# Optimization experiments

Hardware: AMD Instinct MI355X
Metric: run time of the kernel (lower is better)

Reference implementation:

```python
import jax, jax.numpy as jnp
import numpy as np

N = 50000
E = 800000
IN_C, HID_C, OUT_C = 128, 256, 2


def sage_conv(x, src, dst, W_l, b_l, W_r, num_nodes):
    # PyG SAGEConv with mean aggregation:
    #   out = lin_l(mean_{j in N(i)} x_j) + lin_r(x_i)
    msg = x[src]                                            # [E, d] gather
    agg = jax.ops.segment_sum(msg, dst, num_segments=num_nodes)   # [N, d]
    cnt = jax.ops.segment_sum(jnp.ones((msg.shape[0],), x.dtype), dst,
                              num_segments=num_nodes)        # [N]
    agg = agg / jnp.maximum(cnt, 1.0)[:, None]               # mean (deg>=1)
    return agg @ W_l.T + b_l + x @ W_r.T


def setup_inputs() -> dict:
    key = jax.random.key(0)
    ks = jax.random.split(key, 8)
    x = jax.random.normal(ks[0], (N, IN_C), dtype=jnp.float32)
    edge_index = jax.random.randint(ks[1], (2, E), 0, N, dtype=jnp.int32)
    # glorot-ish scaled params
    s1 = 1.0 / np.sqrt(IN_C)
    s2 = 1.0 / np.sqrt(HID_C)
    W1l = jax.random.normal(ks[2], (HID_C, IN_C), dtype=jnp.float32) * s1
    W1r = jax.random.normal(ks[3], (HID_C, IN_C), dtype=jnp.float32) * s1
    b1 = jnp.zeros((HID_C,), dtype=jnp.float32)
    W2l = jax.random.normal(ks[4], (OUT_C, HID_C), dtype=jnp.float32) * s2
    W2r = jax.random.normal(ks[5], (OUT_C, HID_C), dtype=jnp.float32) * s2
    b2 = jnp.zeros((OUT_C,), dtype=jnp.float32)
    return {"x": x, "edge_index": edge_index,
            "W1l": W1l, "b1": b1, "W1r": W1r,
            "W2l": W2l, "b2": b2, "W2r": W2r}


def reference(x, edge_index, W1l, b1, W1r, W2l, b2, W2r):
    src, dst = edge_index[0], edge_index[1]
    h = sage_conv(x, src, dst, W1l, b1, W1r, N)
    h = jax.nn.relu(h)
    out = sage_conv(h, src, dst, W2l, b2, W2r, N)
    return out
```

## Files before the change

### kernel.cpp

```cpp
#include <hip/hip_runtime.h>
#include <hip/hip_bf16.h>


#define IN_C 128
#define HID_C 256
#define BKT_SHIFT 7
#define BKT_W 128
#define CAP 3072

typedef __attribute__((ext_vector_type(8))) short short8;
typedef __attribute__((ext_vector_type(4))) float f32x4;

static __device__ __forceinline__ unsigned short f2b(float f) {
    __hip_bfloat16 h = __float2bfloat16(f);
    return *(unsigned short*)&h;
}
static __device__ __forceinline__ float b2f(unsigned short u) {
    unsigned v = ((unsigned)u) << 16;
    return *(float*)&v;
}

__global__ __launch_bounds__(512) void scatter_conv(
    const float* __restrict__ x, unsigned int* __restrict__ xh,
    unsigned int* __restrict__ Abf,
    const float* __restrict__ w1l, const float* __restrict__ w1r,
    unsigned short* __restrict__ Bg,
    const int* __restrict__ ei, int* __restrict__ bcnt,
    unsigned int* __restrict__ binned,
    int npairs , int xblk, int E_) {
    __shared__ int hist[512];
    __shared__ int lbase[512];
    const int tid = threadIdx.x;
    if (blockIdx.x < xblk) {
        int t = blockIdx.x * 512 + tid;
        if (t >= npairs) return;
        float2 v = *(const float2*)&x[(size_t)t * 2];
        unsigned int o = ((unsigned)f2b(v.y) << 16) | f2b(v.x);
        xh[t] = o;
        int node = t >> 6, g = t & 63;
        Abf[(size_t)node * 128 + 64 + g] = o;
    } else if (blockIdx.x < xblk + 128) {
        int idx = (blockIdx.x - xblk) * 512 + tid;
        int o = idx >> 8, k = idx & 255;
        float f = (k < IN_C) ? w1l[o * IN_C + k] : w1r[o * IN_C + (k - IN_C)];
        Bg[idx] = f2b(f);
    } else {
        const int e0 = (blockIdx.x - xblk - 128) * 2048;
        hist[tid] = 0;
        __syncthreads();
#pragma unroll
        for (int j = 0; j < 4; ++j) {
            int e = e0 + j * 512 + tid;
            if (e < E_) atomicAdd(&hist[ei[E_ + e] >> BKT_SHIFT], 1);
        }
        __syncthreads();
        {
            int c = hist[tid];
            lbase[tid] = c ? tid * CAP + atomicAdd(&bcnt[tid], c) : 0;
            hist[tid] = 0;
        }
        __syncthreads();
#pragma unroll
        for (int j = 0; j < 4; ++j) {
            int e = e0 + j * 512 + tid;
            if (e < E_) {
                int d = ei[E_ + e];
                int b = d >> BKT_SHIFT;
                int pos = lbase[b] + atomicAdd(&hist[b], 1);
                if (pos < b * CAP + CAP)
                    binned[pos] = ((unsigned)ei[e] << BKT_SHIFT) |
                                  (unsigned)(d & (BKT_W - 1));
            }
        }
    }
}


__global__ __launch_bounds__(1024) void sort_gather(
    const unsigned int* __restrict__ binned, const int* __restrict__ bcnt,
    const uint4* __restrict__ xh4, uint4* __restrict__ Abf4,
    int* __restrict__ deg, int n) {
    __shared__ unsigned int ebuf[CAP];
    __shared__ unsigned short sbuf[CAP];
    __shared__ int hist[BKT_W];
    __shared__ int offs[BKT_W];
    __shared__ int cur[BKT_W];
    const int tid = threadIdx.x;
    const int lane = tid & 63;
    const int bkt = blockIdx.x;
    const int gbase = bkt * CAP;
    int cnt = bcnt[bkt];
    if (cnt > CAP) cnt = CAP;

    if (tid < BKT_W) hist[tid] = 0;
    for (int i = tid; i < cnt; i += 1024) ebuf[i] = binned[gbase + i];
    __syncthreads();
    for (int i = tid; i < cnt; i += 1024)
        atomicAdd(&hist[ebuf[i] & (BKT_W - 1)], 1);
    __syncthreads();
    if (tid < 64) {
        int h0 = hist[lane * 2], h1 = hist[lane * 2 + 1];
        int s = h0 + h1;
        int incl = s;
#pragma unroll
        for (int off = 1; off < 64; off <<= 1) {
            int t = __shfl_up(incl, off);
            if (lane >= off) incl += t;
        }
        int excl = incl - s;
        offs[lane * 2] = excl;          cur[lane * 2] = excl;
        offs[lane * 2 + 1] = excl + h0; cur[lane * 2 + 1] = excl + h0;
    }
    __syncthreads();
    for (int i = tid; i < cnt; i += 1024) {
        unsigned int pk = ebuf[i];
        int pos = atomicAdd(&cur[pk & (BKT_W - 1)], 1);
        sbuf[pos] = (unsigned short)(pk >> BKT_SHIFT);
    }
    if (tid < BKT_W) {
        int node = bkt * BKT_W + tid;
        if (node < n) deg[node] = hist[tid];
    }
    __syncthreads();

    const int wv = tid >> 6;
    const int ep = lane >> 4;
    const int pos = lane & 15;
    for (int ld = wv * 8; ld < wv * 8 + 8; ++ld) {
        int node = bkt * BKT_W + ld;
        if (node >= n) break;
        int beg = offs[ld], end = offs[ld] + hist[ld];
        float s[8] = {0.f, 0.f, 0.f, 0.f, 0.f, 0.f, 0.f, 0.f};
        for (int e = beg; e < end; e += 8) {
#pragma unroll
            for (int g = 0; g < 2; ++g) {
                int eg = e + g * 4 + ep;
                if (eg < end) {
                    int src = sbuf[eg];
                    uint4 u = xh4[(size_t)src * 16 + pos];
                    s[0] += b2f(u.x & 0xffff); s[1] += b2f(u.x >> 16);
                    s[2] += b2f(u.y & 0xffff); s[3] += b2f(u.y >> 16);
                    s[4] += b2f(u.z & 0xffff); s[5] += b2f(u.z >> 16);
                    s[6] += b2f(u.w & 0xffff); s[7] += b2f(u.w >> 16);
                }
            }
        }
#pragma unroll
        for (int i = 0; i < 8; ++i) {
            s[i] += __shfl_xor(s[i], 16);
            s[i] += __shfl_xor(s[i], 32);
        }
        if (ep == 0) {
            float inv = 1.0f / (float)max(end - beg, 1);
            uint4 o;
            o.x = ((unsigned)f2b(s[1] * inv) << 16) | f2b(s[0] * inv);
            o.y = ((unsigned)f2b(s[3] * inv) << 16) | f2b(s[2] * inv);
            o.z = ((unsigned)f2b(s[5] * inv) << 16) | f2b(s[4] * inv);
            o.w = ((unsigned)f2b(s[7] * inv) << 16) | f2b(s[6] * inv);
            Abf4[(size_t)node * 32 + pos] = o;
        }
    }
}


#define LSTR 72

__global__ __launch_bounds__(256) void gemm1_fused(
    const unsigned short* __restrict__ Abf, const unsigned short* __restrict__ Bg,
    const float* __restrict__ b1, const float* __restrict__ w2l,
    const float* __restrict__ w2r, float* __restrict__ pr_part, int nn) {
    __shared__ short As[128 * LSTR];
    __shared__ short Bs[128 * LSTR];

    const int tid = threadIdx.x;
    const int lane = tid & 63;
    const int wid = tid >> 6;
    const int wm = wid >> 1, wn = wid & 1;
    const int row0 = blockIdx.x * 128;
    const int col0 = blockIdx.y * 128;

    const int srow = tid >> 1;
    const int skc = (tid & 1) * 32;
    int arow = row0 + srow;
    if (arow >= nn) arow = nn - 1;
    const size_t agoff = (size_t)arow * 256 + skc;
    const size_t bgoff = (size_t)(col0 + srow) * 256 + skc;

    f32x4 acc[4][4];
#pragma unroll
    for (int i = 0; i < 4; ++i)
#pragma unroll
        for (int j = 0; j < 4; ++j) acc[i][j] = (f32x4){0.f, 0.f, 0.f, 0.f};

    const int quad = lane >> 4;
    const int l16 = lane & 15;

    for (int k0 = 0; k0 < 256; k0 += 64) {
        const uint4* ga = (const uint4*)(Abf + agoff + k0);
        const uint4* gb = (const uint4*)(Bg + bgoff + k0);
        uint4 va0 = ga[0], va1 = ga[1], va2 = ga[2], va3 = ga[3];
        uint4 vb0 = gb[0], vb1 = gb[1], vb2 = gb[2], vb3 = gb[3];

        __syncthreads();
        uint4* la = (uint4*)&As[srow * LSTR + skc];
        uint4* lb = (uint4*)&Bs[srow * LSTR + skc];
        la[0] = va0; la[1] = va1; la[2] = va2; la[3] = va3;
        lb[0] = vb0; lb[1] = vb1; lb[2] = vb2; lb[3] = vb3;
        __syncthreads();

#pragma unroll
        for (int kb = 0; kb < 2; ++kb) {
            short8 af[4], bf[4];
#pragma unroll
            for (int mt = 0; mt < 4; ++mt)
                af[mt] = *(const short8*)&As[(wm * 64 + mt * 16 + l16) * LSTR + kb * 32 + quad * 8];
#pragma unroll
            for (int nt = 0; nt < 4; ++nt)
                bf[nt] = *(const short8*)&Bs[(wn * 64 + nt * 16 + l16) * LSTR + kb * 32 + quad * 8];
#pragma unroll
            for (int mt = 0; mt < 4; ++mt)
#pragma unroll
                for (int nt = 0; nt < 4; ++nt)
                    acc[mt][nt] = __builtin_amdgcn_mfma_f32_16x16x32_bf16(
                        af[mt], bf[nt], acc[mt][nt], 0, 0, 0);
        }
    }

    const int cbase = col0 + wn * 64 + l16;
    const int cby = blockIdx.y * 2 + wn;
#pragma unroll
    for (int half = 0; half < 2; ++half) {
        const float* wA = half ? w2r : w2l;
        f32x4 part[2][4];
#pragma unroll
        for (int c = 0; c < 2; ++c)
#pragma unroll
            for (int mt = 0; mt < 4; ++mt) part[c][mt] = (f32x4){0.f, 0.f, 0.f, 0.f};
#pragma unroll
        for (int nt = 0; nt < 4; ++nt) {
            const int col = cbase + nt * 16;
            const float bias = b1[col];
            const float w0 = wA[col];
            const float w1 = wA[HID_C + col];
#pragma unroll
            for (int mt = 0; mt < 4; ++mt)
#pragma unroll
                for (int r = 0; r < 4; ++r) {
                    float hv = fmaxf(acc[mt][nt][r] + bias, 0.0f);
                    part[0][mt][r] += hv * w0;
                    part[1][mt][r] += hv * w1;
                }
        }
#pragma unroll
        for (int c = 0; c < 2; ++c)
#pragma unroll
            for (int mt = 0; mt < 4; ++mt)
#pragma unroll
                for (int r = 0; r < 4; ++r)
#pragma unroll
                    for (int m = 1; m < 16; m <<= 1)
                        part[c][mt][r] += __shfl_xor(part[c][mt][r], m);
        if (l16 < 8) {
            const int ch2 = l16 & 1;
            const int mts = l16 >> 1;
#pragma unroll
            for (int r = 0; r < 4; ++r) {
                int row = row0 + wm * 64 + quad * 4 + mts * 16 + r;
                if (row < nn)
                    pr_part[(size_t)row * 16 + cby * 4 + half * 2 + ch2] =
                        part[ch2][mts][r];
            }
        }
    }
}


__global__ void combine2(const float* __restrict__ pr_part,
                         float2* __restrict__ p2, float2* __restrict__ rs, int n) {
    int i = blockIdx.x * 256 + threadIdx.x;
    if (i >= n) return;
    const float4* q = (const float4*)(pr_part + (size_t)i * 16);
    float4 a = q[0], b = q[1], c = q[2], d = q[3];
    p2[i] = make_float2(a.x + b.x + c.x + d.x, a.y + b.y + c.y + d.y);
    rs[i] = make_float2(a.z + b.z + c.z + d.z, a.w + b.w + c.w + d.w);
}

__global__ __launch_bounds__(256) void fin_bucket(
    const unsigned int* __restrict__ binned, const int* __restrict__ bcnt,
    const float2* __restrict__ p2, const float2* __restrict__ rs,
    const int* __restrict__ deg, const float* __restrict__ b2,
    float* __restrict__ out, int n) {
    __shared__ float a0[BKT_W];
    __shared__ float a1[BKT_W];
    const int tid = threadIdx.x;
    const int bkt = blockIdx.x;
    const int gbase = bkt * CAP;
    int cnt = bcnt[bkt];
    if (cnt > CAP) cnt = CAP;
    if (tid < BKT_W) { a0[tid] = 0.0f; a1[tid] = 0.0f; }
    __syncthreads();
    for (int i = tid; i < cnt; i += 256) {
        unsigned pk = binned[gbase + i];
        float2 v = p2[pk >> BKT_SHIFT];
        atomicAdd(&a0[pk & (BKT_W - 1)], v.x);
        atomicAdd(&a1[pk & (BKT_W - 1)], v.y);
    }
    __syncthreads();
    if (tid < BKT_W) {
        int node = bkt * BKT_W + tid;
        if (node < n) {
            float inv = 1.0f / (float)max(deg[node], 1);
            float2 self = rs[node];
            out[node * 2 + 0] = a0[tid] * inv + self.x + b2[0];
            out[node * 2 + 1] = a1[tid] * inv + self.y + b2[1];
        }
    }
}


extern "C" void kernel_launch(void* const* d_in, const int* in_sizes, int n_in,
                              void* d_out, int out_size, void* d_ws, size_t ws_size,
                              hipStream_t stream) {
    const float* x   = (const float*)d_in[0];
    const int*   ei  = (const int*)d_in[1];
    const float* W1l = (const float*)d_in[2];
    const float* b1  = (const float*)d_in[3];
    const float* W1r = (const float*)d_in[4];
    const float* W2l = (const float*)d_in[5];
    const float* b2  = (const float*)d_in[6];
    const float* W2r = (const float*)d_in[7];
    float* out = (float*)d_out;

    const int N_ = in_sizes[0] / IN_C;
    const int E_ = in_sizes[1] / 2;
    const int nbkt = (N_ + BKT_W - 1) / BKT_W;

    char* wsb = (char*)d_ws;
    size_t off = 0;
    auto alloc = [&](size_t bytes) {
        void* ptr = wsb + off;
        off += ((bytes + 15) & ~(size_t)15);
        return ptr;
    };
    unsigned short* Abf = (unsigned short*)alloc((size_t)N_ * 256 * 2);
    unsigned int*   xh  = (unsigned int*)alloc((size_t)N_ * 64 * 4);
    unsigned short* Bg  = (unsigned short*)alloc(256 * 256 * 2);
    float* pr_part = (float*)alloc((size_t)N_ * 16 * 4);
    unsigned int* binned = (unsigned int*)alloc((size_t)(nbkt + 1) * CAP * 4);
    int*   bcnt   = (int*)alloc(512 * 4);
    int*   deg    = (int*)alloc((size_t)N_ * 4);
    float2* p2 = (float2*)alloc((size_t)N_ * 2 * 4);
    float2* rs = (float2*)alloc((size_t)N_ * 2 * 4);

    const int xblk = (N_ * 64 + 511) / 512;
    const int eblk = (E_ + 2047) / 2048;

    hipMemsetAsync(bcnt, 0, 512 * sizeof(int), stream);
    scatter_conv<<<xblk + 128 + eblk, 512, 0, stream>>>(
        x, xh, (unsigned int*)Abf, W1l, W1r, Bg, ei, bcnt, binned,
        N_ * 64, xblk, E_);

    sort_gather<<<nbkt, 1024, 0, stream>>>(binned, bcnt, (const uint4*)xh,
                                           (uint4*)Abf, deg, N_);

    gemm1_fused<<<dim3((N_ + 127) / 128, 2), 256, 0, stream>>>(
        Abf, Bg, b1, W2l, W2r, pr_part, N_);

    combine2<<<(N_ + 255) / 256, 256, 0, stream>>>(pr_part, p2, rs, N_);
    fin_bucket<<<nbkt, 256, 0, stream>>>(binned, bcnt, p2, rs, deg, b2, out, N_);
}
```

Before: 192.7 us.

## Compute full hidden width per block and fold partial-sum combine into GEMM

The GEMM kernel now uses 1024-thread blocks with 16 waves covering all 256 hidden columns for a 128-row tile, instead of two column-half blocks. The per-wave projections onto the two output channels are reduced through shared memory and written directly to p2/rs. This removes the combine2 kernel launch and the pr_part round trip through global memory, and halves redundant A-tile loads. In exchange, blocks are larger and use more LDS, which may reduce occupancy.

```diff
diff --git a/kernel.cpp b/kernel.cpp
--- a/kernel.cpp
+++ b/kernel.cpp
@@ -165,60 +165,66 @@
 
 #define LSTR 72
 
-__global__ __launch_bounds__(256) void gemm1_fused(
+__global__ __launch_bounds__(1024) void gemm1_fused(
     const unsigned short* __restrict__ Abf, const unsigned short* __restrict__ Bg,
     const float* __restrict__ b1, const float* __restrict__ w2l,
-    const float* __restrict__ w2r, float* __restrict__ pr_part, int nn) {
+    const float* __restrict__ w2r, float2* __restrict__ p2,
+    float2* __restrict__ rs, int nn) {
     __shared__ short As[128 * LSTR];
-    __shared__ short Bs[128 * LSTR];
+    __shared__ short Bs[256 * LSTR];
+    __shared__ float pbuf[16 * 128];
 
     const int tid = threadIdx.x;
     const int lane = tid & 63;
     const int wid = tid >> 6;
-    const int wm = wid >> 1, wn = wid & 1;
+    const int wm = wid >> 2, wn = wid & 3;
     const int row0 = blockIdx.x * 128;
-    const int col0 = blockIdx.y * 128;
-
-    const int srow = tid >> 1;
-    const int skc = (tid & 1) * 32;
-    int arow = row0 + srow;
-    if (arow >= nn) arow = nn - 1;
-    const size_t agoff = (size_t)arow * 256 + skc;
-    const size_t bgoff = (size_t)(col0 + srow) * 256 + skc;
-
-    f32x4 acc[4][4];
-#pragma unroll
-    for (int i = 0; i < 4; ++i)
-#pragma unroll
-        for (int j = 0; j < 4; ++j) acc[i][j] = (f32x4){0.f, 0.f, 0.f, 0.f};
-
     const int quad = lane >> 4;
     const int l16 = lane & 15;
 
+    f32x4 acc[2][4];
+#pragma unroll
+    for (int i = 0; i < 2; ++i)
+#pragma unroll
+        for (int j = 0; j < 4; ++j) acc[i][j] = (f32x4){0.f, 0.f, 0.f, 0.f};
+
     for (int k0 = 0; k0 < 256; k0 += 64) {
-        const uint4* ga = (const uint4*)(Abf + agoff + k0);
-        const uint4* gb = (const uint4*)(Bg + bgoff + k0);
-        uint4 va0 = ga[0], va1 = ga[1], va2 = ga[2], va3 = ga[3];
-        uint4 vb0 = gb[0], vb1 = gb[1], vb2 = gb[2], vb3 = gb[3];
-
-        __syncthreads();
-        uint4* la = (uint4*)&As[srow * LSTR + skc];
-        uint4* lb = (uint4*)&Bs[srow * LSTR + skc];
-        la[0] = va0; la[1] = va1; la[2] = va2; la[3] = va3;
-        lb[0] = vb0; lb[1] = vb1; lb[2] = vb2; lb[3] = vb3;
+        uint4 v[3];
+        int cr[3], ck[3], cb[3];
+#pragma unroll
+        for (int i = 0; i < 3; ++i) {
+            int c = tid + i * 1024;
+            if (c < 1024) {
+                int r = c >> 3;
+                int arow = row0 + r; if (arow >= nn) arow = nn - 1;
+                cr[i] = r; ck[i] = (c & 7) * 8; cb[i] = 0;
+                v[i] = *(const uint4*)(Abf + (size_t)arow * 256 + k0 + ck[i]);
+            } else {
+                int c2 = c - 1024;
+                int r = c2 >> 3;
+                cr[i] = r; ck[i] = (c2 & 7) * 8; cb[i] = 1;
+                v[i] = *(const uint4*)(Bg + (size_t)r * 256 + k0 + ck[i]);
+            }
+        }
+        __syncthreads();
+#pragma unroll
+        for (int i = 0; i < 3; ++i) {
+            short* dst = cb[i] ? &Bs[cr[i] * LSTR + ck[i]] : &As[cr[i] * LSTR + ck[i]];
+            *(uint4*)dst = v[i];
+        }
         __syncthreads();
 
 #pragma unroll
         for (int kb = 0; kb < 2; ++kb) {
-            short8 af[4], bf[4];
-#pragma unroll
-            for (int mt = 0; mt < 4; ++mt)
-                af[mt] = *(const short8*)&As[(wm * 64 + mt * 16 + l16) * LSTR + kb * 32 + quad * 8];
+            short8 af[2], bf[4];
+#pragma unroll
+            for (int mt = 0; mt < 2; ++mt)
+                af[mt] = *(const short8*)&As[(wm * 32 + mt * 16 + l16) * LSTR + kb * 32 + quad * 8];
 #pragma unroll
             for (int nt = 0; nt < 4; ++nt)
                 bf[nt] = *(const short8*)&Bs[(wn * 64 + nt * 16 + l16) * LSTR + kb * 32 + quad * 8];
 #pragma unroll
-            for (int mt = 0; mt < 4; ++mt)
+            for (int mt = 0; mt < 2; ++mt)
 #pragma unroll
                 for (int nt = 0; nt < 4; ++nt)
                     acc[mt][nt] = __builtin_amdgcn_mfma_f32_16x16x32_bf16(
@@ -226,16 +232,15 @@
         }
     }
 
-    const int cbase = col0 + wn * 64 + l16;
-    const int cby = blockIdx.y * 2 + wn;
+    const int cbase = wn * 64 + l16;
 #pragma unroll
     for (int half = 0; half < 2; ++half) {
         const float* wA = half ? w2r : w2l;
-        f32x4 part[2][4];
+        f32x4 part[2][2];
 #pragma unroll
         for (int c = 0; c < 2; ++c)
 #pragma unroll
-            for (int mt = 0; mt < 4; ++mt) part[c][mt] = (f32x4){0.f, 0.f, 0.f, 0.f};
+            for (int mt = 0; mt < 2; ++mt) part[c][mt] = (f32x4){0.f, 0.f, 0.f, 0.f};
 #pragma unroll
         for (int nt = 0; nt < 4; ++nt) {
             const int col = cbase + nt * 16;
@@ -243,7 +248,7 @@
             const float w0 = wA[col];
             const float w1 = wA[HID_C + col];
 #pragma unroll
-            for (int mt = 0; mt < 4; ++mt)
+            for (int mt = 0; mt < 2; ++mt)
 #pragma unroll
                 for (int r = 0; r < 4; ++r) {
                     float hv = fmaxf(acc[mt][nt][r] + bias, 0.0f);
@@ -254,36 +259,39 @@
 #pragma unroll
         for (int c = 0; c < 2; ++c)
 #pragma unroll
-            for (int mt = 0; mt < 4; ++mt)
+            for (int mt = 0; mt < 2; ++mt)
 #pragma unroll
                 for (int r = 0; r < 4; ++r)
 #pragma unroll
                     for (int m = 1; m < 16; m <<= 1)
                         part[c][mt][r] += __shfl_xor(part[c][mt][r], m);
-        if (l16 < 8) {
+        if (l16 < 4) {
             const int ch2 = l16 & 1;
             const int mts = l16 >> 1;
+            const int ch = half * 2 + ch2;
 #pragma unroll
             for (int r = 0; r < 4; ++r) {
-                int row = row0 + wm * 64 + quad * 4 + mts * 16 + r;
-                if (row < nn)
-                    pr_part[(size_t)row * 16 + cby * 4 + half * 2 + ch2] =
-                        part[ch2][mts][r];
+                int row = wm * 32 + mts * 16 + quad * 4 + r;
+                pbuf[(ch * 4 + wn) * 128 + row] = part[ch2][mts][r];
             }
         }
     }
-}
-
-
-__global__ void combine2(const float* __restrict__ pr_part,
-                         float2* __restrict__ p2, float2* __restrict__ rs, int n) {
-    int i = blockIdx.x * 256 + threadIdx.x;
-    if (i >= n) return;
-    const float4* q = (const float4*)(pr_part + (size_t)i * 16);
-    float4 a = q[0], b = q[1], c = q[2], d = q[3];
-    p2[i] = make_float2(a.x + b.x + c.x + d.x, a.y + b.y + c.y + d.y);
-    rs[i] = make_float2(a.z + b.z + c.z + d.z, a.w + b.w + c.w + d.w);
-}
+    __syncthreads();
+
+    if (tid < 128) {
+        int node = row0 + tid;
+        if (node < nn) {
+            float s[4];
+#pragma unroll
+            for (int ch = 0; ch < 4; ++ch)
+                s[ch] = pbuf[(ch * 4 + 0) * 128 + tid] + pbuf[(ch * 4 + 1) * 128 + tid]
+                      + pbuf[(ch * 4 + 2) * 128 + tid] + pbuf[(ch * 4 + 3) * 128 + tid];
+            p2[node] = make_float2(s[0], s[1]);
+            rs[node] = make_float2(s[2], s[3]);
+        }
+    }
+}
+
 
 __global__ __launch_bounds__(256) void fin_bucket(
     const unsigned int* __restrict__ binned, const int* __restrict__ bcnt,
@@ -345,7 +353,6 @@
     unsigned short* Abf = (unsigned short*)alloc((size_t)N_ * 256 * 2);
     unsigned int*   xh  = (unsigned int*)alloc((size_t)N_ * 64 * 4);
     unsigned short* Bg  = (unsigned short*)alloc(256 * 256 * 2);
-    float* pr_part = (float*)alloc((size_t)N_ * 16 * 4);
     unsigned int* binned = (unsigned int*)alloc((size_t)(nbkt + 1) * CAP * 4);
     int*   bcnt   = (int*)alloc(512 * 4);
     int*   deg    = (int*)alloc((size_t)N_ * 4);
@@ -363,9 +370,8 @@
     sort_gather<<<nbkt, 1024, 0, stream>>>(binned, bcnt, (const uint4*)xh,
                                            (uint4*)Abf, deg, N_);
 
-    gemm1_fused<<<dim3((N_ + 127) / 128, 2), 256, 0, stream>>>(
-        Abf, Bg, b1, W2l, W2r, pr_part, N_);
-
-    combine2<<<(N_ + 255) / 256, 256, 0, stream>>>(pr_part, p2, rs, N_);
+    gemm1_fused<<<(N_ + 127) / 128, 1024, 0, stream>>>(
+        Abf, Bg, b1, W2l, W2r, p2, rs, N_);
+
     fin_bucket<<<nbkt, 256, 0, stream>>>(binned, bcnt, p2, rs, deg, b2, out, N_);
 }
```

After: 200.2 us. +3.9%, slower.

## Fuse combine2 into gemm1 via in-block reduction and last-block atomic finalize

Applied to the files above, without the earlier changes.

Partial layer-2 projections are now reduced across the two warp columns in shared memory, and each block writes a compact 8-float-per-node partial instead of 16. A per-row-tile atomic counter lets the second y-block finish the cross-block sum and write p2/rs directly, which removes the separate combine2 launch and halves the partial-buffer traffic. In exchange it adds a threadfence, an atomic and an extra syncthreads plus shared buffer to the gemm epilogue, and it relies on the memset of a larger counter region.

```diff
diff --git a/kernel.cpp b/kernel.cpp
--- a/kernel.cpp
+++ b/kernel.cpp
@@ -168,9 +168,13 @@
 __global__ __launch_bounds__(256) void gemm1_fused(
     const unsigned short* __restrict__ Abf, const unsigned short* __restrict__ Bg,
     const float* __restrict__ b1, const float* __restrict__ w2l,
-    const float* __restrict__ w2r, float* __restrict__ pr_part, int nn) {
+    const float* __restrict__ w2r, float* __restrict__ gpart,
+    int* __restrict__ rcnt, float2* __restrict__ p2, float2* __restrict__ rs,
+    int nn) {
     __shared__ short As[128 * LSTR];
     __shared__ short Bs[128 * LSTR];
+    __shared__ float pbuf[8 * 128];
+    __shared__ int last_s;
 
     const int tid = threadIdx.x;
     const int lane = tid & 63;
@@ -227,7 +231,6 @@
     }
 
     const int cbase = col0 + wn * 64 + l16;
-    const int cby = blockIdx.y * 2 + wn;
 #pragma unroll
     for (int half = 0; half < 2; ++half) {
         const float* wA = half ? w2r : w2l;
@@ -263,27 +266,44 @@
         if (l16 < 8) {
             const int ch2 = l16 & 1;
             const int mts = l16 >> 1;
+            const int ch = half * 2 + ch2;
 #pragma unroll
             for (int r = 0; r < 4; ++r) {
-                int row = row0 + wm * 64 + quad * 4 + mts * 16 + r;
-                if (row < nn)
-                    pr_part[(size_t)row * 16 + cby * 4 + half * 2 + ch2] =
-                        part[ch2][mts][r];
+                int lrow = wm * 64 + mts * 16 + quad * 4 + r;
+                pbuf[(ch * 2 + wn) * 128 + lrow] = part[ch2][mts][r];
             }
         }
     }
-}
-
-
-__global__ void combine2(const float* __restrict__ pr_part,
-                         float2* __restrict__ p2, float2* __restrict__ rs, int n) {
-    int i = blockIdx.x * 256 + threadIdx.x;
-    if (i >= n) return;
-    const float4* q = (const float4*)(pr_part + (size_t)i * 16);
-    float4 a = q[0], b = q[1], c = q[2], d = q[3];
-    p2[i] = make_float2(a.x + b.x + c.x + d.x, a.y + b.y + c.y + d.y);
-    rs[i] = make_float2(a.z + b.z + c.z + d.z, a.w + b.w + c.w + d.w);
-}
+    __syncthreads();
+
+    if (tid < 128) {
+        int node = row0 + tid;
+        if (node < nn) {
+            float4 v;
+            v.x = pbuf[0 * 128 + tid] + pbuf[1 * 128 + tid];
+            v.y = pbuf[2 * 128 + tid] + pbuf[3 * 128 + tid];
+            v.z = pbuf[4 * 128 + tid] + pbuf[5 * 128 + tid];
+            v.w = pbuf[6 * 128 + tid] + pbuf[7 * 128 + tid];
+            *(float4*)&gpart[((size_t)node * 2 + blockIdx.y) * 4] = v;
+        }
+    }
+    __threadfence();
+    if (tid == 0) last_s = atomicAdd(&rcnt[blockIdx.x], 1);
+    __syncthreads();
+    if (last_s == 1) {
+        __threadfence();
+        if (tid < 128) {
+            int node = row0 + tid;
+            if (node < nn) {
+                float4 a = *(const float4*)&gpart[(size_t)node * 8];
+                float4 b = *(const float4*)&gpart[(size_t)node * 8 + 4];
+                p2[node] = make_float2(a.x + b.x, a.y + b.y);
+                rs[node] = make_float2(a.z + b.z, a.w + b.w);
+            }
+        }
+    }
+}
+
 
 __global__ __launch_bounds__(256) void fin_bucket(
     const unsigned int* __restrict__ binned, const int* __restrict__ bcnt,
@@ -345,17 +365,19 @@
     unsigned short* Abf = (unsigned short*)alloc((size_t)N_ * 256 * 2);
     unsigned int*   xh  = (unsigned int*)alloc((size_t)N_ * 64 * 4);
     unsigned short* Bg  = (unsigned short*)alloc(256 * 256 * 2);
-    float* pr_part = (float*)alloc((size_t)N_ * 16 * 4);
+    float* gpart = (float*)alloc((size_t)N_ * 8 * 4);
     unsigned int* binned = (unsigned int*)alloc((size_t)(nbkt + 1) * CAP * 4);
-    int*   bcnt   = (int*)alloc(512 * 4);
-    int*   deg    = (int*)alloc((size_t)N_ * 4);
+    int*   ctrs  = (int*)alloc(1024 * 4);
+    int*   deg   = (int*)alloc((size_t)N_ * 4);
     float2* p2 = (float2*)alloc((size_t)N_ * 2 * 4);
     float2* rs = (float2*)alloc((size_t)N_ * 2 * 4);
+    int* bcnt = ctrs;
+    int* rcnt = ctrs + 512;
 
     const int xblk = (N_ * 64 + 511) / 512;
     const int eblk = (E_ + 2047) / 2048;
 
-    hipMemsetAsync(bcnt, 0, 512 * sizeof(int), stream);
+    hipMemsetAsync(ctrs, 0, 1024 * sizeof(int), stream);
     scatter_conv<<<xblk + 128 + eblk, 512, 0, stream>>>(
         x, xh, (unsigned int*)Abf, W1l, W1r, Bg, ei, bcnt, binned,
         N_ * 64, xblk, E_);
@@ -364,8 +386,7 @@
                                            (uint4*)Abf, deg, N_);
 
     gemm1_fused<<<dim3((N_ + 127) / 128, 2), 256, 0, stream>>>(
-        Abf, Bg, b1, W2l, W2r, pr_part, N_);
-
-    combine2<<<(N_ + 255) / 256, 256, 0, stream>>>(pr_part, p2, rs, N_);
+        Abf, Bg, b1, W2l, W2r, gpart, rcnt, p2, rs, N_);
+
     fin_bucket<<<nbkt, 256, 0, stream>>>(binned, bcnt, p2, rs, deg, b2, out, N_);
 }
```

Result: slower. 306.4 us (+59.0%).
